# Performance work log

Hardware: AMD Instinct MI355X
Metric: run time of the kernel (lower is better)

## Reference

```python
import jax, jax.numpy as jnp
import numpy as np

B, T, C, H, MAX_LEN = 16, 512, 1024, 16, 512
D = C // H  # head_dim = 64

def setup_inputs() -> dict:
    key = jax.random.key(0)
    ks = jax.random.split(key, 10)
    s = 1.0 / np.sqrt(C)
    return {
        "x": jax.random.normal(ks[0], (B, T, C), dtype=jnp.float32),
        "Wq": jax.random.normal(ks[1], (C, C), dtype=jnp.float32) * s,
        "bq": jnp.zeros((C,), dtype=jnp.float32),
        "Wk": jax.random.normal(ks[2], (C, C), dtype=jnp.float32) * s,
        "bk": jnp.zeros((C,), dtype=jnp.float32),
        "Wv": jax.random.normal(ks[3], (C, C), dtype=jnp.float32) * s,
        "bv": jnp.zeros((C,), dtype=jnp.float32),
        "Wo": jax.random.normal(ks[4], (C, C), dtype=jnp.float32) * s,
        "bo": jnp.zeros((C,), dtype=jnp.float32),
        "rel_pos_bias": jax.random.normal(ks[5], (H, MAX_LEN, MAX_LEN), dtype=jnp.float32) * 0.02,
    }

def reference(x, Wq, bq, Wk, bk, Wv, bv, Wo, bo, rel_pos_bias):
    scale = 1.0 / jnp.sqrt(jnp.float32(D))
    # projections (torch Linear: x @ W.T + b), reshape to (B,H,T,D)
    def proj(W, b):
        return (x @ W.T + b).reshape(B, T, H, D).transpose(0, 2, 1, 3)
    q, k, v = proj(Wq, bq), proj(Wk, bk), proj(Wv, bv)
    attn = jnp.einsum('bhtd,bhsd->bhts', q, k) * scale  # (B,H,T,T)
    attn = attn + rel_pos_bias[None, :, :T, :T]
    causal = jnp.triu(jnp.ones((T, T), dtype=bool), k=1)
    attn = jnp.where(causal[None, None], -jnp.inf, attn)
    attn = jax.nn.softmax(attn, axis=-1)  # dropout p=0 (eval) -> identity
    out = jnp.einsum('bhts,bhsd->bhtd', attn, v)
    out = out.transpose(0, 2, 1, 3).reshape(B, T, C)
    return out @ Wo.T + bo
```

## Files before the change

### kernel.cpp

```cpp
#include <hip/hip_runtime.h>
#include <stdint.h>
#include <math.h>

#define DEV static __device__ __forceinline__

typedef __attribute__((ext_vector_type(8))) __bf16 bf16x8;
typedef __attribute__((ext_vector_type(4))) float f32x4;
typedef unsigned short u16;

DEV u16 f2b(float f) {
  union { float f; uint32_t u; } x; x.f = f;
  uint32_t r = x.u + 0x7fffu + ((x.u >> 16) & 1u);
  return (u16)(r >> 16);
}

DEV uint32_t pk2(float a, float b) {
  return (uint32_t)f2b(a) | ((uint32_t)f2b(b) << 16);
}

DEV float b2f_lo(uint32_t u) { return __uint_as_float(u << 16); }
DEV float b2f_hi(uint32_t u) { return __uint_as_float(u & 0xffff0000u); }

DEV void glds16(const void* g, void* l) {
  __builtin_amdgcn_global_load_lds(
      (const __attribute__((address_space(1))) void*)g,
      (__attribute__((address_space(3))) void*)l, 16, 0, 0);
}

DEV f32x4 mfma16(bf16x8 a, bf16x8 b, f32x4 c) {
  return __builtin_amdgcn_mfma_f32_16x16x32_bf16(a, b, c, 0, 0, 0);
}

#define BAR() __builtin_amdgcn_s_barrier()
#define WAIT_LGKM()                                      \
  {                                                      \
    asm volatile("s_waitcnt lgkmcnt(0)" ::: "memory");   \
    __builtin_amdgcn_sched_barrier(0);                   \
  }
#define WAIT_VM4() asm volatile("s_waitcnt vmcnt(4)" ::: "memory")
#define WAIT_VM0() asm volatile("s_waitcnt vmcnt(0)" ::: "memory")

__global__ __launch_bounds__(256) void cvt_all(
    const float* __restrict__ x, const float* __restrict__ Wq,
    const float* __restrict__ Wk, const float* __restrict__ Wv,
    const float* __restrict__ Wo, const float* __restrict__ bias,
    u16* __restrict__ xb, u16* __restrict__ wqkv, u16* __restrict__ wo,
    u16* __restrict__ biasb) {
  size_t i = ((size_t)blockIdx.x * 256 + threadIdx.x) * 4;
  const float* s;
  u16* d;
  size_t off;
  float scale = 1.0f;
  if (i < 8388608)        { s = x;  d = xb;             off = i; }
  else if (i < 9437184)   { s = Wq; d = wqkv;           off = i - 8388608; }
  else if (i < 10485760)  { s = Wk; d = wqkv + 1048576; off = i - 9437184; }
  else if (i < 11534336)  { s = Wv; d = wqkv + 2097152; off = i - 10485760; }
  else if (i < 12582912)  { s = Wo; d = wo;             off = i - 11534336; }
  else { s = bias; d = biasb; off = i - 12582912; scale = 1.44269504f; }
  float4 v = *(const float4*)(s + off);
  ushort4 o;
  o.x = f2b(v.x * scale); o.y = f2b(v.y * scale);
  o.z = f2b(v.z * scale); o.w = f2b(v.w * scale);
  *(ushort4*)(d + off) = o;
}


DEV void stage_a(const u16* A, int m0, int kt, int kh, int wave, int srow,
                 int scol, u16 (*lsA)[2][8192]) {
  const u16* src =
      A + (size_t)(m0 + wave * 32 + srow) * 1024 + kt * 64 + kh * 32 + scol;
  glds16(src, &lsA[kt & 1][kh][wave * 1024]);
  glds16(src + (size_t)16 * 1024, &lsA[kt & 1][kh][wave * 1024 + 512]);
}

DEV void stage_b(const u16* Bw, int n0, int kt, int kh, int wave, int srow,
                 int scol, u16 (*lsB)[2][4096]) {
  glds16(Bw + (size_t)(n0 + wave * 16 + srow) * 1024 + kt * 64 + kh * 32 + scol,
         &lsB[kt & 1][kh][wave * 512]);
}

DEV void load_frags(const u16* Rbase, const u16* Cbase, int wr, int wc,
                    int c16, int swz, bf16x8 rf[4], bf16x8 cf[4]) {
#pragma unroll
  for (int i = 0; i < 4; ++i)
    rf[i] = *(const bf16x8*)&Rbase[(wr * 64 + i * 16 + c16) * 32 + swz];
#pragma unroll
  for (int i = 0; i < 4; ++i)
    cf[i] = *(const bf16x8*)&Cbase[(wc * 64 + i * 16 + c16) * 32 + swz];
}

template <int ILO>
DEV void mfma_half(bf16x8 rf[4], bf16x8 cf[4], f32x4 acc[4][4]) {
  __builtin_amdgcn_s_setprio(1);
#pragma unroll
  for (int j = 0; j < 4; ++j) acc[ILO][j] = mfma16(rf[ILO], cf[j], acc[ILO][j]);
#pragma unroll
  for (int j = 0; j < 4; ++j)
    acc[ILO + 1][j] = mfma16(rf[ILO + 1], cf[j], acc[ILO + 1][j]);
  __builtin_amdgcn_s_setprio(0);
}

DEV void gemm_core(const u16* A, const u16* Bw, int m0, int n0, bool vblk,
                   int wave, int lane, u16 (*lsA)[2][8192],
                   u16 (*lsB)[2][4096], f32x4 acc[4][4]) {
  int q16 = lane >> 4, c16 = lane & 15;
  int wm = wave >> 1, wn = wave & 1;
  int wr = vblk ? wn : wm, wc = vblk ? wm : wn;
  int srow = lane >> 2;
  int scol = ((lane & 3) ^ ((lane >> 3) & 3)) * 8;
  int swz = (q16 ^ ((c16 >> 1) & 3)) * 8;

  stage_a(A, m0, 0, 0, wave, srow, scol, lsA);
  stage_a(A, m0, 0, 1, wave, srow, scol, lsA);
  stage_b(Bw, n0, 0, 0, wave, srow, scol, lsB);
  stage_b(Bw, n0, 0, 1, wave, srow, scol, lsB);
  stage_a(A, m0, 1, 0, wave, srow, scol, lsA);
  stage_a(A, m0, 1, 1, wave, srow, scol, lsA);
  WAIT_VM4();
  BAR();

  bf16x8 rf0[4], rf1[4], cf0[4], cf1[4];
  for (int j = 0; j < 8; ++j) {
    int t = 2 * j;
    const u16* R00 = vblk ? &lsB[0][0][0] : &lsA[0][0][0];
    const u16* C00 = vblk ? &lsA[0][0][0] : &lsB[0][0][0];
    const u16* R01 = vblk ? &lsB[0][1][0] : &lsA[0][1][0];
    const u16* C01 = vblk ? &lsA[0][1][0] : &lsB[0][1][0];
    const u16* R10 = vblk ? &lsB[1][0][0] : &lsA[1][0][0];
    const u16* C10 = vblk ? &lsA[1][0][0] : &lsB[1][0][0];
    const u16* R11 = vblk ? &lsB[1][1][0] : &lsA[1][1][0];
    const u16* C11 = vblk ? &lsA[1][1][0] : &lsB[1][1][0];
    load_frags(R00, C00, wr, wc, c16, swz, rf0, cf0);
    stage_b(Bw, n0, t + 1, 0, wave, srow, scol, lsB);
    BAR();
    WAIT_LGKM();
    mfma_half<0>(rf0, cf0, acc);
    BAR();
    load_frags(R01, C01, wr, wc, c16, swz, rf1, cf1);
    stage_b(Bw, n0, t + 1, 1, wave, srow, scol, lsB);
    BAR();
    WAIT_LGKM();
    mfma_half<2>(rf0, cf0, acc);
    BAR();
    if (j < 7) stage_a(A, m0, t + 2, 0, wave, srow, scol, lsA);
    BAR();
    WAIT_LGKM();
    mfma_half<0>(rf1, cf1, acc);
    BAR();
    if (j < 7) stage_a(A, m0, t + 2, 1, wave, srow, scol, lsA);
    BAR();
    WAIT_LGKM();
    mfma_half<2>(rf1, cf1, acc);
    if (j < 7) { WAIT_VM4(); } else { WAIT_VM0(); }
    BAR();
    load_frags(R10, C10, wr, wc, c16, swz, rf0, cf0);
    if (j < 7) stage_b(Bw, n0, t + 2, 0, wave, srow, scol, lsB);
    BAR();
    WAIT_LGKM();
    mfma_half<0>(rf0, cf0, acc);
    BAR();
    load_frags(R11, C11, wr, wc, c16, swz, rf1, cf1);
    if (j < 7) stage_b(Bw, n0, t + 2, 1, wave, srow, scol, lsB);
    BAR();
    WAIT_LGKM();
    mfma_half<2>(rf0, cf0, acc);
    BAR();
    if (j < 7) stage_a(A, m0, t + 3, 0, wave, srow, scol, lsA);
    BAR();
    WAIT_LGKM();
    mfma_half<0>(rf1, cf1, acc);
    BAR();
    if (j < 7) stage_a(A, m0, t + 3, 1, wave, srow, scol, lsA);
    BAR();
    WAIT_LGKM();
    mfma_half<2>(rf1, cf1, acc);
    if (j < 7) { WAIT_VM4(); } else { WAIT_VM0(); }
    BAR();
  }
}

__global__ __launch_bounds__(512, 2) void gemm_qkv(
    const u16* __restrict__ A, const u16* __restrict__ Bw,
    const float* __restrict__ bq, const float* __restrict__ bk,
    const float* __restrict__ bv,
    u16* __restrict__ qo, u16* __restrict__ ko, u16* __restrict__ vto) {
  __shared__ u16 lsA[2][2][8192];
  __shared__ u16 lsB[2][2][4096];
  int tid = threadIdx.x, wave = tid >> 6, lane = tid & 63;
  int q16 = lane >> 4, c16 = lane & 15;
  int m0 = blockIdx.y * 256, n0 = blockIdx.x * 128;
  int wm = wave >> 1, wn = wave & 1;
  const bool vblk = (n0 >= 2048);

  f32x4 acc[4][4];
#pragma unroll
  for (int i = 0; i < 4; ++i)
#pragma unroll
    for (int j = 0; j < 4; ++j) acc[i][j] = (f32x4)0.0f;

  gemm_core(A, Bw, m0, n0, vblk, wave, lane, lsA, lsB, acc);

  if (!vblk) {
#pragma unroll
    for (int mt = 0; mt < 4; ++mt) {
#pragma unroll
      for (int nt = 0; nt < 4; ++nt) {
        int n = n0 + wn * 64 + nt * 16 + c16;
        int which = n >> 10;
        int nl = n & 1023;
        int hh = nl >> 6, d = nl & 63;
        float bias = (which == 0 ? bq : bk)[nl];
        u16* dst = (which == 0 ? qo : ko);
#pragma unroll
        for (int r = 0; r < 4; ++r) {
          int m = m0 + wm * 64 + mt * 16 + q16 * 4 + r;
          int b = m >> 9, t = m & 511;
          size_t bh = (size_t)b * 16 + hh;
          dst[(bh * 512 + t) * 72 + d] = f2b(acc[mt][nt][r] + bias);
        }
      }
    }
  } else {
#pragma unroll
    for (int it = 0; it < 4; ++it) {
      int nbase = n0 + wn * 64 + it * 16 + q16 * 4;
      float4 bvv = *(const float4*)(bv + (nbase & 1023));
#pragma unroll
      for (int jt = 0; jt < 4; ++jt) {
        int m = m0 + wm * 64 + jt * 16 + c16;
        int b = m >> 9, t = m & 511;
        size_t bh4 = ((size_t)b * 16) * 4;
#pragma unroll
        for (int r = 0; r < 4; ++r) {
          int nl = (nbase + r) & 1023;
          int hh = nl >> 6, d = nl & 63;
          float bias = ((const float*)&bvv)[r];
          vto[((bh4 + (size_t)hh * 4 + (t >> 7)) * 64 + d) * 136 + (t & 127)] =
              f2b(acc[it][jt][r] + bias);
        }
      }
    }
  }
}

__global__ __launch_bounds__(256, 3) void attn_kernel(
    const u16* __restrict__ qglob, const u16* __restrict__ kglob,
    const u16* __restrict__ vtglob, const u16* __restrict__ biasb,
    u16* __restrict__ og) {
  __shared__ u16 lsK[128 * 72];
  __shared__ u16 lsV[64 * 136];
  __shared__ u16 lsP[4 * 32 * 72];

  int tid = threadIdx.x, wave = tid >> 6, lane = tid & 63;
  int q16 = lane >> 4, c16 = lane & 15;
  u16* lsPw = lsP + wave * (32 * 72);

  int p = blockIdx.x;
  int bx, bh, bx2 = -1, bh2 = 0;
  if (p < 256)      { bx = 3; bh = p; }
  else if (p < 512) { bx = 2; bh = p - 256; bx2 = 0; bh2 = p - 256; }
  else              { int q = p - 512; bx = 1; bh = 2 * q; bx2 = 1; bh2 = 2 * q + 1; }

  for (;;) {
    int b = bh >> 4, h = bh & 15;
    int q0 = bx * 128;

    const u16* qbase = qglob + (size_t)bh * (512 * 72) + (size_t)q0 * 72;
    const u16* kbase = kglob + (size_t)bh * (512 * 72);
    const u16* vbase = vtglob + (size_t)bh * 4 * (64 * 136);

    for (int i = wave; i < 18; i += 4)
      glds16(qbase + (size_t)i * 512 + lane * 8, lsK + i * 512);
    __syncthreads();
    bf16x8 qf[2][2];
#pragma unroll
    for (int nt = 0; nt < 2; ++nt)
#pragma unroll
      for (int ks = 0; ks < 2; ++ks)
        qf[nt][ks] = *(const bf16x8*)&lsK[(wave * 32 + nt * 16 + c16) * 72 +
                                          ks * 32 + q16 * 8];

    f32x4 oacc[2][4];
#pragma unroll
    for (int i = 0; i < 2; ++i)
#pragma unroll
      for (int j = 0; j < 4; ++j) oacc[i][j] = (f32x4)0.0f;
    float mold[2] = {-INFINITY, -INFINITY};
    float lsum[2] = {0.0f, 0.0f};
    const float SCL = 0.18033688f;

    for (int st = 0; st <= bx; ++st) {
      bool diag = (st == bx);
      __syncthreads();
      const u16* kt = kbase + (size_t)st * (128 * 72);
      for (int i = wave; i < 18; i += 4)
        glds16(kt + (size_t)i * 512 + lane * 8, lsK + i * 512);
      const u16* vt = vbase + (size_t)st * (64 * 136);
      for (int i = wave; i < 17; i += 4)
        glds16(vt + (size_t)i * 512 + lane * 8, lsV + i * 512);

      uint2 ub[2][8];
#pragma unroll
      for (int nt = 0; nt < 2; ++nt) {
        int qgl = q0 + wave * 32 + nt * 16 + c16;
        const u16* bp =
            biasb + ((size_t)h * 512 + qgl) * 512 + st * 128 + q16 * 4;
#pragma unroll
        for (int mt = 0; mt < 8; ++mt) ub[nt][mt] = *(const uint2*)(bp + mt * 16);
      }
      __syncthreads();

      f32x4 sa[8][2];
#pragma unroll
      for (int mt = 0; mt < 8; ++mt) {
        sa[mt][0] = (f32x4)0.0f;
        sa[mt][1] = (f32x4)0.0f;
      }
      int mtmax = diag ? 2 * wave + 2 : 8;
#pragma unroll
      for (int mt = 0; mt < 8; ++mt) {
        if (mt < mtmax) {
#pragma unroll
          for (int ks = 0; ks < 2; ++ks) {
            bf16x8 kf =
                *(const bf16x8*)&lsK[(mt * 16 + c16) * 72 + ks * 32 + q16 * 8];
            sa[mt][0] = mfma16(kf, qf[0][ks], sa[mt][0]);
            sa[mt][1] = mfma16(kf, qf[1][ks], sa[mt][1]);
          }
        }
      }

      float alpha[2];
#pragma unroll
      for (int nt = 0; nt < 2; ++nt) {
#pragma unroll
        for (int mt = 0; mt < 8; ++mt) {
          uint32_t lo = ub[nt][mt].x, hi = ub[nt][mt].y;
          f32x4 bv;
          bv[0] = b2f_lo(lo); bv[1] = b2f_hi(lo);
          bv[2] = b2f_lo(hi); bv[3] = b2f_hi(hi);
          sa[mt][nt] = sa[mt][nt] * SCL + bv;
        }
        if (diag) {
#pragma unroll
          for (int mt = 0; mt < 8; ++mt) {
            int d0 = mt * 16 + q16 * 4 - wave * 32 - nt * 16 - c16;
#pragma unroll
            for (int r = 0; r < 4; ++r)
              if (d0 + r > 0) sa[mt][nt][r] = -INFINITY;
          }
        }
        f32x4 m4 = sa[0][nt];
#pragma unroll
        for (int mt = 1; mt < 8; ++mt) {
          f32x4 v = sa[mt][nt];
          m4[0] = fmaxf(m4[0], v[0]); m4[1] = fmaxf(m4[1], v[1]);
          m4[2] = fmaxf(m4[2], v[2]); m4[3] = fmaxf(m4[3], v[3]);
        }
        float mx = fmaxf(fmaxf(m4[0], m4[1]), fmaxf(m4[2], m4[3]));
        mx = fmaxf(mx, __shfl_xor(mx, 16));
        mx = fmaxf(mx, __shfl_xor(mx, 32));
        float mnew = fmaxf(mold[nt], mx);
        alpha[nt] = exp2f(mold[nt] - mnew);
        mold[nt] = mnew;
        f32x4 s4 = (f32x4)0.0f;
#pragma unroll
        for (int mt = 0; mt < 8; ++mt) {
          f32x4 pq;
          pq[0] = exp2f(sa[mt][nt][0] - mnew);
          pq[1] = exp2f(sa[mt][nt][1] - mnew);
          pq[2] = exp2f(sa[mt][nt][2] - mnew);
          pq[3] = exp2f(sa[mt][nt][3] - mnew);
          sa[mt][nt] = pq;
          s4 += pq;
        }
        float ss = (s4[0] + s4[1]) + (s4[2] + s4[3]);
        ss += __shfl_xor(ss, 16);
        ss += __shfl_xor(ss, 32);
        lsum[nt] = lsum[nt] * alpha[nt] + ss;
      }

#pragma unroll
      for (int mo = 0; mo < 2; ++mo) {
        f32x4 av;
#pragma unroll
        for (int r = 0; r < 4; ++r) av[r] = __shfl(alpha[mo], q16 * 4 + r);
#pragma unroll
        for (int dt = 0; dt < 4; ++dt) oacc[mo][dt] *= av;
      }

      int G = diag ? wave + 1 : 4;
#pragma unroll
      for (int hf = 0; hf < 2; ++hf) {
        if (hf * 2 < G) {
#pragma unroll
          for (int nt = 0; nt < 2; ++nt)
#pragma unroll
            for (int mt4 = 0; mt4 < 4; ++mt4) {
              f32x4 pv = sa[hf * 4 + mt4][nt];
              uint2 w;
              w.x = pk2(pv[0], pv[1]);
              w.y = pk2(pv[2], pv[3]);
              *(uint2*)&lsPw[(nt * 16 + c16) * 72 + mt4 * 16 + q16 * 4] = w;
            }
#pragma unroll
          for (int ksh = 0; ksh < 2; ++ksh) {
            if (hf * 2 + ksh < G) {
              bf16x8 pf0 =
                  *(const bf16x8*)&lsPw[c16 * 72 + ksh * 32 + q16 * 8];
              bf16x8 pf1 =
                  *(const bf16x8*)&lsPw[(16 + c16) * 72 + ksh * 32 + q16 * 8];
#pragma unroll
              for (int dt = 0; dt < 4; ++dt) {
                bf16x8 vf = *(const bf16x8*)&lsV[(dt * 16 + c16) * 136 +
                                                 hf * 64 + ksh * 32 + q16 * 8];
                oacc[0][dt] = mfma16(pf0, vf, oacc[0][dt]);
                oacc[1][dt] = mfma16(pf1, vf, oacc[1][dt]);
              }
            }
          }
        }
      }
    }

#pragma unroll
    for (int mo = 0; mo < 2; ++mo) {
      f32x4 lv;
#pragma unroll
      for (int r = 0; r < 4; ++r) lv[r] = __shfl(lsum[mo], q16 * 4 + r);
#pragma unroll
      for (int r = 0; r < 4; ++r) {
        int tg = q0 + wave * 32 + mo * 16 + q16 * 4 + r;
        float inv = 1.0f / lv[r];
#pragma unroll
        for (int dt = 0; dt < 4; ++dt)
          og[((size_t)b * 512 + tg) * 1024 + h * 64 + dt * 16 + c16] =
              f2b(oacc[mo][dt][r] * inv);
      }
    }

    if (bx2 < 0) break;
    __syncthreads();
    bx = bx2; bh = bh2; bx2 = -1;
  }
}

__global__ __launch_bounds__(512, 2) void gemm_out(
    const u16* __restrict__ A, const u16* __restrict__ W,
    const float* __restrict__ bo, float* __restrict__ out) {
  __shared__ u16 lsA[2][2][8192];
  __shared__ u16 lsB[2][2][4096];
  int tid = threadIdx.x, wave = tid >> 6, lane = tid & 63;
  int q16 = lane >> 4, c16 = lane & 15;
  int m0 = blockIdx.y * 256, n0 = blockIdx.x * 128;
  int wm = wave >> 1, wn = wave & 1;

  f32x4 acc[4][4];
#pragma unroll
  for (int i = 0; i < 4; ++i)
#pragma unroll
    for (int j = 0; j < 4; ++j) acc[i][j] = (f32x4)0.0f;

  gemm_core(A, W, m0, n0, false, wave, lane, lsA, lsB, acc);

#pragma unroll
  for (int mt = 0; mt < 4; ++mt) {
#pragma unroll
    for (int nt = 0; nt < 4; ++nt) {
      int n = n0 + wn * 64 + nt * 16 + c16;
      float bias = bo[n];
#pragma unroll
      for (int r = 0; r < 4; ++r) {
        int m = m0 + wm * 64 + mt * 16 + q16 * 4 + r;
        out[(size_t)m * 1024 + n] = acc[mt][nt][r] + bias;
      }
    }
  }
}

extern "C" void kernel_launch(void* const* d_in, const int* in_sizes, int n_in,
                              void* d_out, int out_size, void* d_ws, size_t ws_size,
                              hipStream_t stream) {
  const float* x    = (const float*)d_in[0];
  const float* Wq   = (const float*)d_in[1];
  const float* bq   = (const float*)d_in[2];
  const float* Wk   = (const float*)d_in[3];
  const float* bk   = (const float*)d_in[4];
  const float* Wv   = (const float*)d_in[5];
  const float* bv   = (const float*)d_in[6];
  const float* Wo   = (const float*)d_in[7];
  const float* bo   = (const float*)d_in[8];
  const float* bias = (const float*)d_in[9];
  float* out = (float*)d_out;

  const size_t MB = 1u << 20;
  char* ws = (char*)d_ws;
  u16* xb    = (u16*)(ws);
  u16* wqkv  = (u16*)(ws + 16 * MB);
  u16* wo    = (u16*)(ws + 22 * MB);
  u16* biasb = (u16*)(ws + 24 * MB);
  u16* qb    = (u16*)(ws + 32 * MB);
  u16* kb    = (u16*)(ws + 50 * MB);
  u16* vtb   = (u16*)(ws + 68 * MB);
  u16* ab    = xb;

  cvt_all<<<16384, 256, 0, stream>>>(x, Wq, Wk, Wv, Wo, bias,
                                     xb, wqkv, wo, biasb);
  gemm_qkv<<<dim3(24, 32), 512, 0, stream>>>(xb, wqkv, bq, bk, bv, qb, kb, vtb);
  attn_kernel<<<dim3(640), 256, 0, stream>>>(qb, kb, vtb, biasb, ab);
  gemm_out<<<dim3(8, 32), 512, 0, stream>>>(ab, wo, bo, out);
}
```

Before: 286.8 us.

## Restructure GEMM main loop into four-phase pipeline with fewer barriers

Replaces the eight-sub-phase-per-tile GEMM loop, which issued separate A and B staging and a barrier after each half MFMA block, with a four-phase scheme. Each phase loads fragments for one k-half, stages both A and B for a future k-half, then runs all sixteen MFMAs before one vmcnt wait. The prologue now prefetches three k-halves instead of two, and vmcnt thresholds are retuned to match. This cuts barrier and waitcnt overhead and lengthens MFMA bursts, at the cost of tighter LDS buffer-reuse correctness and a different overlap pattern.

```diff
diff --git a/kernel.cpp b/kernel.cpp
--- a/kernel.cpp
+++ b/kernel.cpp
@@ -37,7 +37,8 @@
     asm volatile("s_waitcnt lgkmcnt(0)" ::: "memory");   \
     __builtin_amdgcn_sched_barrier(0);                   \
   }
-#define WAIT_VM4() asm volatile("s_waitcnt vmcnt(4)" ::: "memory")
+#define WAIT_VM6() asm volatile("s_waitcnt vmcnt(6)" ::: "memory")
+#define WAIT_VM3() asm volatile("s_waitcnt vmcnt(3)" ::: "memory")
 #define WAIT_VM0() asm volatile("s_waitcnt vmcnt(0)" ::: "memory")
 
 __global__ __launch_bounds__(256) void cvt_all(
@@ -89,16 +90,31 @@
     cf[i] = *(const bf16x8*)&Cbase[(wc * 64 + i * 16 + c16) * 32 + swz];
 }
 
-template <int ILO>
-DEV void mfma_half(bf16x8 rf[4], bf16x8 cf[4], f32x4 acc[4][4]) {
-  __builtin_amdgcn_s_setprio(1);
-#pragma unroll
-  for (int j = 0; j < 4; ++j) acc[ILO][j] = mfma16(rf[ILO], cf[j], acc[ILO][j]);
-#pragma unroll
-  for (int j = 0; j < 4; ++j)
-    acc[ILO + 1][j] = mfma16(rf[ILO + 1], cf[j], acc[ILO + 1][j]);
-  __builtin_amdgcn_s_setprio(0);
-}
+DEV void mfma_all(bf16x8 rf[4], bf16x8 cf[4], f32x4 acc[4][4]) {
+#pragma unroll
+  for (int i = 0; i < 4; ++i)
+#pragma unroll
+    for (int j = 0; j < 4; ++j) acc[i][j] = mfma16(rf[i], cf[j], acc[i][j]);
+}
+
+#define GPH(BUF, KH, DOST, STT, STKH, VMW)                                 \
+  {                                                                        \
+    const u16* Rb = vblk ? &lsB[BUF][KH][0] : &lsA[BUF][KH][0];            \
+    const u16* Cb = vblk ? &lsA[BUF][KH][0] : &lsB[BUF][KH][0];            \
+    bf16x8 rf[4], cf[4];                                                   \
+    load_frags(Rb, Cb, wr, wc, c16, swz, rf, cf);                          \
+    if (DOST) {                                                            \
+      stage_a(A, m0, (STT), (STKH), wave, srow, scol, lsA);                \
+      stage_b(Bw, n0, (STT), (STKH), wave, srow, scol, lsB);               \
+    }                                                                      \
+    BAR();                                                                 \
+    WAIT_LGKM();                                                           \
+    __builtin_amdgcn_s_setprio(1);                                         \
+    mfma_all(rf, cf, acc);                                                 \
+    __builtin_amdgcn_s_setprio(0);                                         \
+    VMW;                                                                   \
+    BAR();                                                                 \
+  }
 
 DEV void gemm_core(const u16* A, const u16* Bw, int m0, int n0, bool vblk,
                    int wave, int lane, u16 (*lsA)[2][8192],
@@ -111,72 +127,24 @@
   int swz = (q16 ^ ((c16 >> 1) & 3)) * 8;
 
   stage_a(A, m0, 0, 0, wave, srow, scol, lsA);
+  stage_b(Bw, n0, 0, 0, wave, srow, scol, lsB);
   stage_a(A, m0, 0, 1, wave, srow, scol, lsA);
-  stage_b(Bw, n0, 0, 0, wave, srow, scol, lsB);
   stage_b(Bw, n0, 0, 1, wave, srow, scol, lsB);
   stage_a(A, m0, 1, 0, wave, srow, scol, lsA);
-  stage_a(A, m0, 1, 1, wave, srow, scol, lsA);
-  WAIT_VM4();
+  stage_b(Bw, n0, 1, 0, wave, srow, scol, lsB);
+  WAIT_VM6();
   BAR();
 
-  bf16x8 rf0[4], rf1[4], cf0[4], cf1[4];
-  for (int j = 0; j < 8; ++j) {
-    int t = 2 * j;
-    const u16* R00 = vblk ? &lsB[0][0][0] : &lsA[0][0][0];
-    const u16* C00 = vblk ? &lsA[0][0][0] : &lsB[0][0][0];
-    const u16* R01 = vblk ? &lsB[0][1][0] : &lsA[0][1][0];
-    const u16* C01 = vblk ? &lsA[0][1][0] : &lsB[0][1][0];
-    const u16* R10 = vblk ? &lsB[1][0][0] : &lsA[1][0][0];
-    const u16* C10 = vblk ? &lsA[1][0][0] : &lsB[1][0][0];
-    const u16* R11 = vblk ? &lsB[1][1][0] : &lsA[1][1][0];
-    const u16* C11 = vblk ? &lsA[1][1][0] : &lsB[1][1][0];
-    load_frags(R00, C00, wr, wc, c16, swz, rf0, cf0);
-    stage_b(Bw, n0, t + 1, 0, wave, srow, scol, lsB);
-    BAR();
-    WAIT_LGKM();
-    mfma_half<0>(rf0, cf0, acc);
-    BAR();
-    load_frags(R01, C01, wr, wc, c16, swz, rf1, cf1);
-    stage_b(Bw, n0, t + 1, 1, wave, srow, scol, lsB);
-    BAR();
-    WAIT_LGKM();
-    mfma_half<2>(rf0, cf0, acc);
-    BAR();
-    if (j < 7) stage_a(A, m0, t + 2, 0, wave, srow, scol, lsA);
-    BAR();
-    WAIT_LGKM();
-    mfma_half<0>(rf1, cf1, acc);
-    BAR();
-    if (j < 7) stage_a(A, m0, t + 2, 1, wave, srow, scol, lsA);
-    BAR();
-    WAIT_LGKM();
-    mfma_half<2>(rf1, cf1, acc);
-    if (j < 7) { WAIT_VM4(); } else { WAIT_VM0(); }
-    BAR();
-    load_frags(R10, C10, wr, wc, c16, swz, rf0, cf0);
-    if (j < 7) stage_b(Bw, n0, t + 2, 0, wave, srow, scol, lsB);
-    BAR();
-    WAIT_LGKM();
-    mfma_half<0>(rf0, cf0, acc);
-    BAR();
-    load_frags(R11, C11, wr, wc, c16, swz, rf1, cf1);
-    if (j < 7) stage_b(Bw, n0, t + 2, 1, wave, srow, scol, lsB);
-    BAR();
-    WAIT_LGKM();
-    mfma_half<2>(rf0, cf0, acc);
-    BAR();
-    if (j < 7) stage_a(A, m0, t + 3, 0, wave, srow, scol, lsA);
-    BAR();
-    WAIT_LGKM();
-    mfma_half<0>(rf1, cf1, acc);
-    BAR();
-    if (j < 7) stage_a(A, m0, t + 3, 1, wave, srow, scol, lsA);
-    BAR();
-    WAIT_LGKM();
-    mfma_half<2>(rf1, cf1, acc);
-    if (j < 7) { WAIT_VM4(); } else { WAIT_VM0(); }
-    BAR();
-  }
+  for (int j = 0; j < 7; ++j) {
+    GPH(0, 0, true, 2 * j + 1, 1, WAIT_VM6());
+    GPH(0, 1, true, 2 * j + 2, 0, WAIT_VM6());
+    GPH(1, 0, true, 2 * j + 2, 1, WAIT_VM6());
+    GPH(1, 1, true, 2 * j + 3, 0, WAIT_VM6());
+  }
+  GPH(0, 0, true, 15, 1, WAIT_VM6());
+  GPH(0, 1, false, 0, 0, WAIT_VM3());
+  GPH(1, 0, false, 0, 0, WAIT_VM0());
+  GPH(1, 1, false, 0, 0, );
 }
 
 __global__ __launch_bounds__(512, 2) void gemm_qkv(
```

Result: faster. 279.3 us (-2.6%).
